# Kernel tuning notes

Measured on AMD Instinct MI355X. Metric: run time of the kernel, lower is better.

Reference implementation:

```python
import jax, jax.numpy as jnp
import numpy as np

# FP4 E2M1 constants (from the torch module)
EXP_BITS = 2
EXP_BIAS = 1          # 2**(EXP_BITS-1) - 1
MANT_BITS = 1
MAX_EXP_FIELD = 3     # (1 << EXP_BITS) - 1
MIN_NORMAL_EXP = 0    # 1 - EXP_BIAS
FP4_MAX = 6.0         # (1 + 1/2) * 2**(MAX_EXP_FIELD-1 - EXP_BIAS + 1) = 1.5 * 4
GROUP = 128


def fp4_quant_dequant(x):
    """Faithful composition of _float_to_fp4 followed by _fp4_to_float (E2M1,
    subnormal-aware), expressed in float arithmetic (bit pack/unpack cancels)."""
    a = jnp.abs(x)
    zero_mask = a == 0
    a_safe = jnp.where(zero_mask, jnp.float32(1e-8), a)
    e = jnp.floor(jnp.log2(a_safe))                      # unbiased exponent
    is_sub = e < MIN_NORMAL_EXP
    e_c = jnp.clip(e, MIN_NORMAL_EXP, MAX_EXP_FIELD - EXP_BIAS)
    mant_scale = float(1 << MANT_BITS)                   # 2.0
    mant_normal = jnp.clip(jnp.round((a_safe / jnp.exp2(e_c) - 1.0) * mant_scale), 0.0, mant_scale - 1.0)
    mant_sub = jnp.clip(jnp.round(a_safe / (2.0 ** MIN_NORMAL_EXP) * mant_scale), 0.0, mant_scale - 1.0)
    mant = jnp.where(is_sub, mant_sub, mant_normal)
    # decode (_fp4_to_float): normals (1 + m/2)*2^(e), subnormals (m/2)*2^(1-bias)
    val_normal = (1.0 + mant / mant_scale) * jnp.exp2(e_c)
    val_sub = (mant / mant_scale) * (2.0 ** (1 - EXP_BIAS))
    val = jnp.where(is_sub, val_sub, val_normal)
    val = jnp.where(x < 0, -val, val)
    return jnp.where(zero_mask, jnp.zeros_like(val), val)


def setup_inputs() -> dict:
    key = jax.random.key(0)
    k1, k2, k3 = jax.random.split(key, 3)
    x = jax.random.normal(k1, (4096, 4096), dtype=jnp.float32)
    weight = jax.random.normal(k2, (4096, 4096), dtype=jnp.float32) * 0.02
    b = jax.random.normal(k3, (4096,), dtype=jnp.float32)
    return {"x": x, "weight": weight, "b": b}


def reference(x, weight, b):
    out_f, in_f = weight.shape
    wg = weight.reshape(out_f, in_f // GROUP, GROUP)
    amax = jnp.max(jnp.abs(wg), axis=-1, keepdims=True)       # [out, groups, 1]
    scale = jnp.where(amax == 0, jnp.float32(1.0), amax / FP4_MAX)
    w_deq = (fp4_quant_dequant(wg / scale) * scale).reshape(out_f, in_f)
    return x @ w_deq.T + b
```

## Files before the change

### kernel.cpp

```cpp
#include <hip/hip_runtime.h>
#include <hip/hip_bf16.h>
#include <stdint.h>

#define KDIM 4096
#define NDIM 4096
#define MDIM 4096
#define BM 256
#define BN 256
#define BK 64

typedef __attribute__((ext_vector_type(8))) short bf16x8;
typedef __attribute__((ext_vector_type(4))) float f32x4;


__device__ __forceinline__ unsigned short bf16bits(float f) {
    union { float f; uint32_t u; } c; c.f = f;
    uint32_t u = c.u;
    uint32_t r = (u + 0x7fffu + ((u >> 16) & 1u)) >> 16;
    return (unsigned short)r;
}

__device__ __forceinline__ float fp4qd(float x) {
    float a = fabsf(x);
    if (a == 0.0f) return 0.0f;
    float e = floorf(log2f(a));
    float val;
    if (e < 0.0f) {
        float mant = fminf(fmaxf(rintf(a * 2.0f), 0.0f), 1.0f);
        val = mant * 0.5f;
    } else {
        float ec = fminf(e, 2.0f);
        float p  = exp2f(ec);
        float mant = fminf(fmaxf(rintf((a / p - 1.0f) * 2.0f), 0.0f), 1.0f);
        val = (1.0f + 0.5f * mant) * p;
    }
    return (x < 0.0f) ? -val : val;
}

__device__ __forceinline__ void gld16(void* lds, const void* g) {
    __builtin_amdgcn_global_load_lds(
        (const __attribute__((address_space(1))) unsigned int*)g,
        (__attribute__((address_space(3))) unsigned int*)lds,
        16, 0, 0);
}

__global__ __launch_bounds__(256) void prep_kernel(const float* __restrict__ X,
                                                   const float* __restrict__ W,
                                                   unsigned short* __restrict__ Xb,
                                                   unsigned short* __restrict__ Wq) {
    int bid = blockIdx.x;
    int tid = threadIdx.x;
    if (bid < 16384) {
        size_t i = ((size_t)bid * 256 + tid) * 4;
        float4 v = *(const float4*)(X + i);
        ushort4 o;
        o.x = bf16bits(v.x); o.y = bf16bits(v.y);
        o.z = bf16bits(v.z); o.w = bf16bits(v.w);
        *(ushort4*)(Xb + i) = o;
    } else {
        size_t base = ((size_t)(bid - 16384) * 256 + tid) * 4;
        float4 v = *(const float4*)(W + base);
        float am = fmaxf(fmaxf(fabsf(v.x), fabsf(v.y)),
                         fmaxf(fabsf(v.z), fabsf(v.w)));
        #pragma unroll
        for (int s = 16; s; s >>= 1) am = fmaxf(am, __shfl_xor(am, s));
        float scale = (am == 0.0f) ? 1.0f : am / 6.0f;
        ushort4 o;
        o.x = bf16bits(fp4qd(v.x / scale) * scale);
        o.y = bf16bits(fp4qd(v.y / scale) * scale);
        o.z = bf16bits(fp4qd(v.z / scale) * scale);
        o.w = bf16bits(fp4qd(v.w / scale) * scale);
        *(ushort4*)(Wq + base) = o;
    }
}


#define BAR()    __builtin_amdgcn_s_barrier()
#define LGKM0()  asm volatile("s_waitcnt lgkmcnt(0)" ::: "memory")
#define VM4()    asm volatile("s_waitcnt vmcnt(4)" ::: "memory")
#define SCH0()   __builtin_amdgcn_sched_barrier(0)
#define PRIO(x)  __builtin_amdgcn_s_setprio(x)

__global__ __launch_bounds__(512, 2) void gemm256(const unsigned short* __restrict__ A,
                                                  const unsigned short* __restrict__ B,
                                                  const float* __restrict__ bias,
                                                  float* __restrict__ C) {
    __shared__ __attribute__((aligned(16))) char smem[2][2][2][16384];
    char* sm = (char*)&smem[0][0][0][0];

    const int t = threadIdx.x;
    const int l = t & 63;
    const int w = __builtin_amdgcn_readfirstlane(t >> 6);
    const int wm = w >> 2;
    const int wn = w & 3;

    int bid = blockIdx.x;
    int swz = (bid & 7) * 32 + (bid >> 3);
    int brow = (swz >> 4) * BM;
    int bcol = (swz & 15) * BN;

    const int lr8  = l >> 3;
    const int slot = l & 7;
    const int scol = (slot ^ lr8) << 3;
    const unsigned short* pA = A + (size_t)(brow + w * 8 + lr8) * KDIM + scol;
    const unsigned short* pB = B + (size_t)(bcol + w * 8 + lr8) * KDIM + scol;

#define STAGE(b, op, h, kt) do {                                               \
    const unsigned short* _s = ((op) ? pB : pA)                                \
        + (size_t)(h) * 128 * KDIM + (size_t)(kt) * BK;                        \
    gld16(sm + (b) * 65536 + (op) * 32768 + (h) * 16384 + w * 1024, _s);       \
    gld16(sm + (b) * 65536 + (op) * 32768 + (h) * 16384 + 8192 + w * 1024,     \
          _s + (size_t)64 * KDIM);                                             \
} while (0)

    const int fr  = l & 15;
    const int fq  = l >> 4;
    const int kx0 = ((fq    ) ^ (fr & 7)) << 4;
    const int kx1 = ((fq + 4) ^ (fr & 7)) << 4;
    const int frA = fr * 128;

#define RD_A(b, mh) do {                                                        \
    const char* _p = sm + (b) * 65536 + wm * 16384 + (mh) * 8192 + frA;         \
    _Pragma("unroll")                                                           \
    for (int m = 0; m < 4; ++m) {                                               \
        av[m][0] = *(const bf16x8*)(_p + m * 2048 + kx0);                       \
        av[m][1] = *(const bf16x8*)(_p + m * 2048 + kx1);                       \
    }                                                                           \
} while (0)

#define RD_B(b, nh, arr) do {                                                   \
    const char* _p = sm + (b) * 65536 + 32768 + wn * 8192 + (nh) * 4096 + frA;  \
    _Pragma("unroll")                                                           \
    for (int n = 0; n < 2; ++n) {                                               \
        arr[n][0] = *(const bf16x8*)(_p + n * 2048 + kx0);                      \
        arr[n][1] = *(const bf16x8*)(_p + n * 2048 + kx1);                      \
    }                                                                           \
} while (0)

#define MM(mh, nh, B_)                                                          \
    _Pragma("unroll")                                                           \
    for (int m = 0; m < 4; ++m)                                                 \
        _Pragma("unroll")                                                       \
        for (int n = 0; n < 2; ++n)                                             \
            _Pragma("unroll")                                                   \
            for (int ks = 0; ks < 2; ++ks)                                      \
                acc[(mh) * 4 + m][(nh) * 2 + n] =                               \
                    __builtin_amdgcn_mfma_f32_16x16x32_bf16(                    \
                        av[m][ks], B_[n][ks], acc[(mh) * 4 + m][(nh) * 2 + n],  \
                        0, 0, 0);

    f32x4 acc[8][4];
    #pragma unroll
    for (int m = 0; m < 8; ++m)
        #pragma unroll
        for (int n = 0; n < 4; ++n)
            acc[m][n] = f32x4{0.f, 0.f, 0.f, 0.f};

    bf16x8 av[4][2], bvA[2][2], bvB[2][2];

    STAGE(0, 0, 0, 0); STAGE(0, 0, 1, 0); STAGE(0, 1, 0, 0); STAGE(0, 1, 1, 0);
    STAGE(1, 1, 0, 1); STAGE(1, 0, 0, 1);
    VM4();
    BAR();
    RD_B(0, 0, bvA);
    SCH0();

    for (int it = 0; it < 32; ++it) {
        const int k1 = 2 * it + 1;
        const int k2 = (2 * it + 2) & 63;
        const int k3 = (2 * it + 3) & 63;

        RD_A(0, 0); STAGE(1, 0, 1, k1);
        BAR(); LGKM0(); SCH0(); PRIO(1); MM(0, 0, bvA); PRIO(0); BAR(); SCH0();
        RD_B(0, 1, bvB); STAGE(1, 1, 1, k1);
        BAR(); LGKM0(); SCH0(); PRIO(1); MM(0, 1, bvB); PRIO(0); BAR(); SCH0();
        RD_A(0, 1); STAGE(0, 1, 0, k2);
        BAR(); LGKM0(); SCH0(); PRIO(1); MM(1, 1, bvB); PRIO(0); BAR(); SCH0();
        STAGE(0, 0, 0, k2);
        BAR(); SCH0(); PRIO(1); MM(1, 0, bvA); PRIO(0);
        VM4(); RD_B(1, 0, bvA);
        BAR(); SCH0();

        RD_A(1, 0); STAGE(0, 0, 1, k2);
        BAR(); LGKM0(); SCH0(); PRIO(1); MM(0, 0, bvA); PRIO(0); BAR(); SCH0();
        RD_B(1, 1, bvB); STAGE(0, 1, 1, k2);
        BAR(); LGKM0(); SCH0(); PRIO(1); MM(0, 1, bvB); PRIO(0); BAR(); SCH0();
        RD_A(1, 1); STAGE(1, 1, 0, k3);
        BAR(); LGKM0(); SCH0(); PRIO(1); MM(1, 1, bvB); PRIO(0); BAR(); SCH0();
        STAGE(1, 0, 0, k3);
        BAR(); SCH0(); PRIO(1); MM(1, 0, bvA); PRIO(0);
        VM4(); RD_B(0, 0, bvA);
        BAR(); SCH0();
    }

    float bb[4];
    #pragma unroll
    for (int n = 0; n < 4; ++n) bb[n] = bias[bcol + wn * 64 + n * 16 + fr];
    #pragma unroll
    for (int mi = 0; mi < 8; ++mi) {
        #pragma unroll
        for (int q = 0; q < 4; ++q) {
            int row = brow + wm * 128 + mi * 16 + fq * 4 + q;
            float* crow = C + (size_t)row * NDIM + bcol + wn * 64;
            #pragma unroll
            for (int n = 0; n < 4; ++n)
                crow[n * 16 + fr] = acc[mi][n][q] + bb[n];
        }
    }
}

extern "C" void kernel_launch(void* const* d_in, const int* in_sizes, int n_in,
                              void* d_out, int out_size, void* d_ws, size_t ws_size,
                              hipStream_t stream) {
    const float* x = (const float*)d_in[0];
    const float* w = (const float*)d_in[1];
    const float* b = (const float*)d_in[2];
    float* out = (float*)d_out;

    unsigned short* xb = (unsigned short*)d_ws;
    unsigned short* wq = xb + (size_t)NDIM * KDIM;

    prep_kernel<<<32768, 256, 0, stream>>>(x, w, xb, wq);
    gemm256<<<(MDIM / BM) * (NDIM / BN), 512, 0, stream>>>(xb, wq, b, out);
}
```

Baseline: 150.0 us.

## Load B fragments directly from global into registers, stage only A in LDS

The B operand is no longer staged through shared memory. Each wave loads its own B MFMA fragments directly from global memory into registers, double-buffered across even and odd k-tiles, and LDS holds only A (64KB instead of 128KB). The pipeline is simplified to one vmcnt(0)+barrier per k-tile instead of the multi-phase interleaved schedule. This removes B LDS traffic and frees LDS, at the cost of uncoalesced 16-byte global loads for B, B being re-read by the two waves that share the same columns, and full vmcnt(0) stalls.

```diff
diff --git a/kernel.cpp b/kernel.cpp
--- a/kernel.cpp
+++ b/kernel.cpp
@@ -77,7 +77,7 @@
 
 #define BAR()    __builtin_amdgcn_s_barrier()
 #define LGKM0()  asm volatile("s_waitcnt lgkmcnt(0)" ::: "memory")
-#define VM4()    asm volatile("s_waitcnt vmcnt(4)" ::: "memory")
+#define VM0()    asm volatile("s_waitcnt vmcnt(0)" ::: "memory")
 #define SCH0()   __builtin_amdgcn_sched_barrier(0)
 #define PRIO(x)  __builtin_amdgcn_s_setprio(x)
 
@@ -85,8 +85,8 @@
                                                   const unsigned short* __restrict__ B,
                                                   const float* __restrict__ bias,
                                                   float* __restrict__ C) {
-    __shared__ __attribute__((aligned(16))) char smem[2][2][2][16384];
-    char* sm = (char*)&smem[0][0][0][0];
+    __shared__ __attribute__((aligned(16))) char smem[2][32768];
+    char* sm = (char*)&smem[0][0];
 
     const int t = threadIdx.x;
     const int l = t & 63;
@@ -103,15 +103,14 @@
     const int slot = l & 7;
     const int scol = (slot ^ lr8) << 3;
     const unsigned short* pA = A + (size_t)(brow + w * 8 + lr8) * KDIM + scol;
-    const unsigned short* pB = B + (size_t)(bcol + w * 8 + lr8) * KDIM + scol;
-
-#define STAGE(b, op, h, kt) do {                                               \
-    const unsigned short* _s = ((op) ? pB : pA)                                \
-        + (size_t)(h) * 128 * KDIM + (size_t)(kt) * BK;                        \
-    gld16(sm + (b) * 65536 + (op) * 32768 + (h) * 16384 + w * 1024, _s);       \
-    gld16(sm + (b) * 65536 + (op) * 32768 + (h) * 16384 + 8192 + w * 1024,     \
+
+#define STAGE_A(b, h, kt) do {                                                 \
+    const unsigned short* _s = pA + (size_t)(h) * 128 * KDIM + (size_t)(kt) * BK; \
+    gld16(sm + (b) * 32768 + (h) * 16384 + w * 1024, _s);                      \
+    gld16(sm + (b) * 32768 + (h) * 16384 + 8192 + w * 1024,                    \
           _s + (size_t)64 * KDIM);                                             \
 } while (0)
+#define STAGE4(b, kt) do { STAGE_A(b, 0, kt); STAGE_A(b, 1, kt); } while (0)
 
     const int fr  = l & 15;
     const int fq  = l >> 4;
@@ -120,7 +119,7 @@
     const int frA = fr * 128;
 
 #define RD_A(b, mh) do {                                                        \
-    const char* _p = sm + (b) * 65536 + wm * 16384 + (mh) * 8192 + frA;         \
+    const char* _p = sm + (b) * 32768 + wm * 16384 + (mh) * 8192 + frA;         \
     _Pragma("unroll")                                                           \
     for (int m = 0; m < 4; ++m) {                                               \
         av[m][0] = *(const bf16x8*)(_p + m * 2048 + kx0);                       \
@@ -128,26 +127,27 @@
     }                                                                           \
 } while (0)
 
-#define RD_B(b, nh, arr) do {                                                   \
-    const char* _p = sm + (b) * 65536 + 32768 + wn * 8192 + (nh) * 4096 + frA;  \
+    const unsigned short* pBg = B + (size_t)(bcol + wn * 64 + fr) * KDIM + fq * 8;
+
+#define GLB_B(arr, kt) do {                                                     \
+    const unsigned short* _b = pBg + (size_t)(kt) * BK;                         \
     _Pragma("unroll")                                                           \
-    for (int n = 0; n < 2; ++n) {                                               \
-        arr[n][0] = *(const bf16x8*)(_p + n * 2048 + kx0);                      \
-        arr[n][1] = *(const bf16x8*)(_p + n * 2048 + kx1);                      \
+    for (int nf = 0; nf < 4; ++nf) {                                            \
+        arr[nf][0] = *(const bf16x8*)(_b + (size_t)(nf * 16) * KDIM);           \
+        arr[nf][1] = *(const bf16x8*)(_b + (size_t)(nf * 16) * KDIM + 32);      \
     }                                                                           \
 } while (0)
 
-#define MM(mh, nh, B_)                                                          \
+#define MMH(mh, B_)                                                             \
     _Pragma("unroll")                                                           \
-    for (int m = 0; m < 4; ++m)                                                 \
+    for (int nf = 0; nf < 4; ++nf)                                              \
         _Pragma("unroll")                                                       \
-        for (int n = 0; n < 2; ++n)                                             \
+        for (int m = 0; m < 4; ++m)                                             \
             _Pragma("unroll")                                                   \
             for (int ks = 0; ks < 2; ++ks)                                      \
-                acc[(mh) * 4 + m][(nh) * 2 + n] =                               \
+                acc[(mh) * 4 + m][nf] =                                         \
                     __builtin_amdgcn_mfma_f32_16x16x32_bf16(                    \
-                        av[m][ks], B_[n][ks], acc[(mh) * 4 + m][(nh) * 2 + n],  \
-                        0, 0, 0);
+                        av[m][ks], B_[nf][ks], acc[(mh) * 4 + m][nf], 0, 0, 0);
 
     f32x4 acc[8][4];
     #pragma unroll
@@ -156,41 +156,34 @@
         for (int n = 0; n < 4; ++n)
             acc[m][n] = f32x4{0.f, 0.f, 0.f, 0.f};
 
-    bf16x8 av[4][2], bvA[2][2], bvB[2][2];
-
-    STAGE(0, 0, 0, 0); STAGE(0, 0, 1, 0); STAGE(0, 1, 0, 0); STAGE(0, 1, 1, 0);
-    STAGE(1, 1, 0, 1); STAGE(1, 0, 0, 1);
-    VM4();
-    BAR();
-    RD_B(0, 0, bvA);
-    SCH0();
+    bf16x8 av[4][2], bEv[4][2], bOd[4][2];
+
+    STAGE4(0, 0);
+    GLB_B(bEv, 0);
 
     for (int it = 0; it < 32; ++it) {
-        const int k1 = 2 * it + 1;
-        const int k2 = (2 * it + 2) & 63;
-        const int k3 = (2 * it + 3) & 63;
-
-        RD_A(0, 0); STAGE(1, 0, 1, k1);
-        BAR(); LGKM0(); SCH0(); PRIO(1); MM(0, 0, bvA); PRIO(0); BAR(); SCH0();
-        RD_B(0, 1, bvB); STAGE(1, 1, 1, k1);
-        BAR(); LGKM0(); SCH0(); PRIO(1); MM(0, 1, bvB); PRIO(0); BAR(); SCH0();
-        RD_A(0, 1); STAGE(0, 1, 0, k2);
-        BAR(); LGKM0(); SCH0(); PRIO(1); MM(1, 1, bvB); PRIO(0); BAR(); SCH0();
-        STAGE(0, 0, 0, k2);
-        BAR(); SCH0(); PRIO(1); MM(1, 0, bvA); PRIO(0);
-        VM4(); RD_B(1, 0, bvA);
-        BAR(); SCH0();
-
-        RD_A(1, 0); STAGE(0, 0, 1, k2);
-        BAR(); LGKM0(); SCH0(); PRIO(1); MM(0, 0, bvA); PRIO(0); BAR(); SCH0();
-        RD_B(1, 1, bvB); STAGE(0, 1, 1, k2);
-        BAR(); LGKM0(); SCH0(); PRIO(1); MM(0, 1, bvB); PRIO(0); BAR(); SCH0();
-        RD_A(1, 1); STAGE(1, 1, 0, k3);
-        BAR(); LGKM0(); SCH0(); PRIO(1); MM(1, 1, bvB); PRIO(0); BAR(); SCH0();
-        STAGE(1, 0, 0, k3);
-        BAR(); SCH0(); PRIO(1); MM(1, 0, bvA); PRIO(0);
-        VM4(); RD_B(0, 0, bvA);
-        BAR(); SCH0();
+        const int kO  = 2 * it + 1;
+        const int kE2 = (2 * it + 2) & 63;
+
+        VM0(); BAR(); SCH0();
+        RD_A(0, 0);
+        GLB_B(bOd, kO);
+        STAGE4(1, kO);
+        LGKM0(); SCH0();
+        PRIO(1); MMH(0, bEv); PRIO(0); SCH0();
+        RD_A(0, 1);
+        LGKM0(); SCH0();
+        PRIO(1); MMH(1, bEv); PRIO(0);
+
+        VM0(); BAR(); SCH0();
+        RD_A(1, 0);
+        GLB_B(bEv, kE2);
+        STAGE4(0, kE2);
+        LGKM0(); SCH0();
+        PRIO(1); MMH(0, bOd); PRIO(0); SCH0();
+        RD_A(1, 1);
+        LGKM0(); SCH0();
+        PRIO(1); MMH(1, bOd); PRIO(0);
     }
 
     float bb[4];
```

Measured after the change: 220.0 us. 46.7% more time.

## Merge GEMM main-loop phases to halve barriers and reorder MFMA loop

Applied to the files above, without the earlier changes.

Restructures the ping-pong main loop: each half-iteration now has two compute phases instead of four. Shared-memory fragment reads and global-to-LDS stages are grouped ahead of a single barrier, and two MFMA blocks run back to back. The MFMA macro's loop nest now puts the k-slice outermost, so consecutive MFMAs hit independent accumulators. This cuts workgroup barriers and wait counts per iteration, but having fewer barriers raises the risk of LDS read/write races between waves and lengthens each phase's register live ranges.

```diff
diff --git a/kernel.cpp b/kernel.cpp
--- a/kernel.cpp
+++ b/kernel.cpp
@@ -139,11 +139,11 @@
 
 #define MM(mh, nh, B_)                                                          \
     _Pragma("unroll")                                                           \
-    for (int m = 0; m < 4; ++m)                                                 \
+    for (int ks = 0; ks < 2; ++ks)                                              \
         _Pragma("unroll")                                                       \
-        for (int n = 0; n < 2; ++n)                                             \
+        for (int m = 0; m < 4; ++m)                                             \
             _Pragma("unroll")                                                   \
-            for (int ks = 0; ks < 2; ++ks)                                      \
+            for (int n = 0; n < 2; ++n)                                         \
                 acc[(mh) * 4 + m][(nh) * 2 + n] =                               \
                     __builtin_amdgcn_mfma_f32_16x16x32_bf16(                    \
                         av[m][ks], B_[n][ks], acc[(mh) * 4 + m][(nh) * 2 + n],  \
@@ -170,27 +170,25 @@
         const int k2 = (2 * it + 2) & 63;
         const int k3 = (2 * it + 3) & 63;
 
-        RD_A(0, 0); STAGE(1, 0, 1, k1);
-        BAR(); LGKM0(); SCH0(); PRIO(1); MM(0, 0, bvA); PRIO(0); BAR(); SCH0();
-        RD_B(0, 1, bvB); STAGE(1, 1, 1, k1);
-        BAR(); LGKM0(); SCH0(); PRIO(1); MM(0, 1, bvB); PRIO(0); BAR(); SCH0();
-        RD_A(0, 1); STAGE(0, 1, 0, k2);
-        BAR(); LGKM0(); SCH0(); PRIO(1); MM(1, 1, bvB); PRIO(0); BAR(); SCH0();
-        STAGE(0, 0, 0, k2);
-        BAR(); SCH0(); PRIO(1); MM(1, 0, bvA); PRIO(0);
+        RD_A(0, 0); RD_B(0, 1, bvB);
+        STAGE(1, 0, 1, k1); STAGE(1, 1, 1, k1);
+        BAR(); LGKM0(); SCH0();
+        PRIO(1); MM(0, 0, bvA); MM(0, 1, bvB); PRIO(0);
+        RD_A(0, 1);
+        STAGE(0, 1, 0, k2); STAGE(0, 0, 0, k2);
+        BAR(); LGKM0(); SCH0();
+        PRIO(1); MM(1, 1, bvB); MM(1, 0, bvA); PRIO(0);
         VM4(); RD_B(1, 0, bvA);
-        BAR(); SCH0();
-
-        RD_A(1, 0); STAGE(0, 0, 1, k2);
-        BAR(); LGKM0(); SCH0(); PRIO(1); MM(0, 0, bvA); PRIO(0); BAR(); SCH0();
-        RD_B(1, 1, bvB); STAGE(0, 1, 1, k2);
-        BAR(); LGKM0(); SCH0(); PRIO(1); MM(0, 1, bvB); PRIO(0); BAR(); SCH0();
-        RD_A(1, 1); STAGE(1, 1, 0, k3);
-        BAR(); LGKM0(); SCH0(); PRIO(1); MM(1, 1, bvB); PRIO(0); BAR(); SCH0();
-        STAGE(1, 0, 0, k3);
-        BAR(); SCH0(); PRIO(1); MM(1, 0, bvA); PRIO(0);
+
+        RD_A(1, 0); RD_B(1, 1, bvB);
+        STAGE(0, 0, 1, k2); STAGE(0, 1, 1, k2);
+        BAR(); LGKM0(); SCH0();
+        PRIO(1); MM(0, 0, bvA); MM(0, 1, bvB); PRIO(0);
+        RD_A(1, 1);
+        STAGE(1, 1, 0, k3); STAGE(1, 0, 0, k3);
+        BAR(); LGKM0(); SCH0();
+        PRIO(1); MM(1, 1, bvB); MM(1, 0, bvA); PRIO(0);
         VM4(); RD_B(0, 0, bvA);
-        BAR(); SCH0();
     }
 
     float bb[4];
```

Result: no change. 148.6 us (-0.9%).
